# Kernel optimization log

Hardware: AMD Instinct MI355X
Metric: run time of the kernel (lower is better)

## Reference

```python
import jax, jax.numpy as jnp
import numpy as np

N, NB, D, F, E, NUM_RBF = 50000, 256, 128, 16, 800000, 15
EPS = 1e-7
NEG = 0.01
MAX_LEN = 5.0


def _glorot(k, shape):
    return jax.random.normal(k, shape, dtype=jnp.float32) / np.float32(np.sqrt(shape[0]))


def setup_inputs() -> dict:
    key = jax.random.key(0)
    ks = jax.random.split(key, 32)
    inp = {}
    inp['h_A'] = jax.random.normal(ks[0], (N, D), jnp.float32)
    inp['v_A'] = jax.random.normal(ks[1], (N, F, 3), jnp.float32)
    inp['x_A'] = jax.random.normal(ks[2], (N, 3), jnp.float32) * 3.0
    inp['h_B'] = jax.random.normal(ks[3], (NB, D), jnp.float32)
    inp['mask'] = jnp.ones((N, NB), jnp.float32)
    inp['src'] = jax.random.randint(ks[4], (E,), 0, N, dtype=jnp.int32)
    inp['dst'] = jax.random.randint(ks[5], (E,), 0, N, dtype=jnp.int32)
    inp['rbf_k'] = jnp.array([0.5], jnp.float32)
    inp['W_rbf1'] = _glorot(ks[6], (NUM_RBF, D)); inp['b_rbf1'] = jnp.zeros((D,), jnp.float32)
    inp['W_rbf2'] = _glorot(ks[7], (NUM_RBF, F)); inp['b_rbf2'] = jnp.zeros((F,), jnp.float32)
    inp['W_rbf3'] = _glorot(ks[8], (NUM_RBF, F)); inp['b_rbf3'] = jnp.zeros((F,), jnp.float32)
    inp['vn1_W'] = _glorot(ks[9], (F, F)); inp['vn1_U'] = _glorot(ks[10], (F, F))
    inp['vn2_W'] = _glorot(ks[11], (F, F)); inp['vn2_U'] = _glorot(ks[12], (F, F))
    inp['vn3_W'] = _glorot(ks[13], (F, F)); inp['vn3_U'] = _glorot(ks[14], (F, F))
    inp['phi1_W'] = _glorot(ks[15], (D + F, D)); inp['phi1_b'] = jnp.zeros((D,), jnp.float32)
    inp['phi2_W'] = _glorot(ks[16], (D + F, F)); inp['phi2_b'] = jnp.zeros((F,), jnp.float32)
    inp['phi3_W'] = _glorot(ks[17], (D, F)); inp['phi3_b'] = jnp.zeros((F,), jnp.float32)
    inp['Wq'] = _glorot(ks[18], (D, D)); inp['Wk'] = _glorot(ks[19], (D, D))
    inp['Wv'] = _glorot(ks[20], (D, D)); inp['bv'] = jnp.zeros((D,), jnp.float32)
    inp['gru_Wih'] = _glorot(ks[21], (3 * D, 2 * D)) * 0.5
    inp['gru_Whh'] = _glorot(ks[22], (3 * D, D)) * 0.5
    inp['gru_bih'] = jnp.zeros((3 * D,), jnp.float32)
    inp['gru_bhh'] = jnp.zeros((3 * D,), jnp.float32)
    inp['vmlp_W1'] = _glorot(ks[23], (2 * F, 2 * F)); inp['vmlp_U1'] = _glorot(ks[24], (2 * F, 2 * F))
    inp['vmlp_W2'] = _glorot(ks[25], (F, 2 * F))
    return inp


def _forward(h_A, v_A, x_A, h_B, mask, src, dst, rbf_k, W_rbf1, b_rbf1, W_rbf2, b_rbf2,
             W_rbf3, b_rbf3, vn1_W, vn1_U, vn2_W, vn2_U, vn3_W, vn3_U, phi1_W, phi1_b,
             phi2_W, phi2_b, phi3_W, phi3_b, Wq, Wk, Wv, bv, gru_Wih, gru_Whh, gru_bih,
             gru_bhh, vmlp_W1, vmlp_U1, vmlp_W2):
    lrelu = lambda x: jax.nn.leaky_relu(x, NEG)

    def vn_relu(v, W, U):  # Vector Neuron linear + VN-ReLU; v: [n, f, 3]
        q = jnp.einsum('gf,nfc->ngc', W, v)
        k = jnp.einsum('gf,nfc->ngc', U, v)
        dot = jnp.sum(q * k, -1, keepdims=True)
        ksq = jnp.sum(k * k, -1, keepdims=True) + EPS
        return jnp.where(dot >= 0, q, q - (dot / ksq) * k)

    # --- per-node mixed scalar/vector features (generate_mixed_features) ---
    vnorm1 = jnp.linalg.norm(vn_relu(v_A, vn1_W, vn1_U), axis=2) + EPS  # [N,F]
    vnorm2 = jnp.linalg.norm(vn_relu(v_A, vn2_W, vn2_U), axis=2) + EPS
    hp = lrelu(jnp.concatenate([h_A, vnorm1], 1) @ phi1_W + phi1_b)     # [N,D]
    hpp = lrelu(jnp.concatenate([h_A, vnorm2], 1) @ phi2_W + phi2_b)    # [N,F]
    vp = vn_relu(v_A, vn3_W, vn3_U) * lrelu(h_A @ phi3_W + phi3_b)[:, :, None]  # [N,F,3]

    # --- cross attention A <- B ---
    q = lrelu(h_A @ Wq)
    kk = lrelu(h_B @ Wk)
    vv = h_B @ Wv + bv
    a = mask * (q @ kk.T) - 1000.0 * (1.0 - mask)                       # [N,NB]
    attn = jax.nn.softmax(a, axis=1) @ vv                               # [N,D]

    # --- edge-wise RBF expansion + point convolution messages ---
    r_ij = x_A[src] - x_A[dst]                                          # [E,3]
    rnorm = jnp.linalg.norm(r_ij, axis=1, keepdims=True)                # [E,1]
    centers = jnp.linspace(0.0, MAX_LEN, NUM_RBF, dtype=jnp.float32)
    rbf = jnp.exp(-jnp.square(rnorm - centers) * rbf_k)                 # [E,R]
    rbf_h = rbf @ W_rbf1 + b_rbf1                                       # [E,D]
    rbf_v1 = rbf @ W_rbf2 + b_rbf2                                      # [E,F]
    rbf_v2 = rbf @ W_rbf3 + b_rbf3                                      # [E,F]
    msg_h = rbf_h * hp[dst]                                             # [E,D]
    # einsum('ef,ef,ec->efc', rbf_v2, hpp_dst, r_ij)
    msg_v = rbf_v1[:, :, None] * vp[dst] + (rbf_v2 * hpp[dst])[:, :, None] * r_ij[:, None, :]

    # --- mean aggregation at destination nodes (update_all copy_e + mean) ---
    n_nodes = h_A.shape[0]
    cnt = jax.ops.segment_sum(jnp.ones((src.shape[0],), msg_h.dtype), dst, num_segments=n_nodes)
    den = jnp.maximum(cnt, 1.0)
    agg_h = jax.ops.segment_sum(msg_h, dst, num_segments=n_nodes) / den[:, None]
    agg_v = jax.ops.segment_sum(msg_v, dst, num_segments=n_nodes) / den[:, None, None]

    # --- GRUCell(2D, D): input = [h, cross_attn], hidden = aggregated message ---
    x_in = jnp.concatenate([h_A, attn], -1)                             # [N,2D]
    gi = x_in @ gru_Wih.T + gru_bih
    gh = agg_h @ gru_Whh.T + gru_bhh
    Dh = h_A.shape[1]
    r = jax.nn.sigmoid(gi[:, :Dh] + gh[:, :Dh])
    z = jax.nn.sigmoid(gi[:, Dh:2 * Dh] + gh[:, Dh:2 * Dh])
    n = jnp.tanh(gi[:, 2 * Dh:] + r * gh[:, 2 * Dh:])
    node_upd = h_A + ((1.0 - z) * n + z * agg_h)

    # --- vector update via Vector_MLP(2F -> F) with residual ---
    vin = jnp.concatenate([v_A, agg_v], axis=1)                         # [N,2F,3]
    vh = vn_relu(vin, vmlp_W1, vmlp_U1)
    v_evolved = v_A + jnp.einsum('gf,nfc->ngc', vmlp_W2, vh)            # [N,F,3]
    return v_evolved, node_upd


def reference(h_A, v_A, x_A, h_B, mask, src, dst, rbf_k, W_rbf1, b_rbf1, W_rbf2, b_rbf2,
              W_rbf3, b_rbf3, vn1_W, vn1_U, vn2_W, vn2_U, vn3_W, vn3_U, phi1_W, phi1_b,
              phi2_W, phi2_b, phi3_W, phi3_b, Wq, Wk, Wv, bv, gru_Wih, gru_Whh, gru_bih,
              gru_bhh, vmlp_W1, vmlp_U1, vmlp_W2):
    return _forward(h_A, v_A, x_A, h_B, mask, src, dst, rbf_k, W_rbf1, b_rbf1, W_rbf2,
                    b_rbf2, W_rbf3, b_rbf3, vn1_W, vn1_U, vn2_W, vn2_U, vn3_W, vn3_U,
                    phi1_W, phi1_b, phi2_W, phi2_b, phi3_W, phi3_b, Wq, Wk, Wv, bv,
                    gru_Wih, gru_Whh, gru_bih, gru_bhh, vmlp_W1, vmlp_U1, vmlp_W2)
```

## Files before the change

kernel.cpp:

```cpp
#include <hip/hip_runtime.h>
#include <math.h>

#define NN 50000
#define NBB 256
#define DD 128
#define FF 16
#define EE 800000
#define RR 15
#define EPSV 1e-7f
#define CSPACE (5.0f/14.0f)

__device__ __forceinline__ float lrelu(float x){ return x >= 0.f ? x : 0.01f*x; }
__device__ __forceinline__ float sigmoidf_(float x){ return 1.f/(1.f+expf(-x)); }

typedef __bf16 bf16x8 __attribute__((ext_vector_type(8)));
typedef float f32x4 __attribute__((ext_vector_type(4)));

__device__ __forceinline__ unsigned short f2bf(float x){
    union { float f; unsigned int u; } a; a.f = x;
    unsigned int r = (a.u + 0x7fffu + ((a.u >> 16) & 1u)) >> 16;
    return (unsigned short)r;
}
__device__ __forceinline__ unsigned int pack2(float a, float b){
    return (unsigned int)f2bf(a) | ((unsigned int)f2bf(b) << 16);
}
__device__ __forceinline__ float bf2f(unsigned short v){
    union { unsigned int u; float f; } a; a.u = ((unsigned int)v) << 16; return a.f;
}
__device__ __forceinline__ bf16x8 ld8(const unsigned short* p){
    union { uint4 u; bf16x8 b; } x; x.u = *(const uint4*)p; return x.b;
}

__global__ void k_prep(const float* __restrict__ Wih, const float* __restrict__ Whh,
                       const float* __restrict__ Wq,
                       const float* __restrict__ phi1W, const float* __restrict__ phi2W,
                       const float* __restrict__ phi3W,
                       const float* __restrict__ Wr1, const float* __restrict__ br1,
                       unsigned short* __restrict__ pWih, unsigned short* __restrict__ pWhh,
                       unsigned short* __restrict__ pWq,
                       unsigned short* __restrict__ pPhi1, unsigned short* __restrict__ pPhi2,
                       unsigned short* __restrict__ pPhi3, unsigned short* __restrict__ pWr1){
    int i = blockIdx.x*256 + threadIdx.x;
    if (i < 3*8*8*64*8){
        int e = i&7, l=(i>>3)&63, kt=(i>>9)&7, c=(i>>12)&7, q=i>>15;
        int row = q*128 + c*16 + (l&15);
        int k = kt*32 + (l>>4)*8 + e;
        pWih[i] = f2bf(Wih[row*256 + k]);
    }
    if (i < 3*8*4*64*8){
        int e = i&7, l=(i>>3)&63, kt=(i>>9)&3, c=(i>>11)&7, q=i>>14;
        int row = q*128 + c*16 + (l&15);
        int k = kt*32 + (l>>4)*8 + e;
        pWhh[i] = f2bf(Whh[row*128 + k]);
    }
    if (i < 8*4*64*8){
        int e = i&7, l=(i>>3)&63, kt=(i>>9)&3, c=(i>>11)&7;
        pWq[i] = f2bf(Wq[(kt*32 + (l>>4)*8 + e)*DD + c*16 + (l&15)]);
    }
    if (i < 8*5*64*8){
        int e = i&7, l=(i>>3)&63;
        int t = i>>9;
        int kt = t%5, c = t/5;
        int k = kt*32 + (l>>4)*8 + e;
        int col = c*16 + (l&15);
        pPhi1[i] = f2bf(k < 144 ? phi1W[k*DD + col] : 0.f);
    }
    if (i < 5*64*8){
        int e = i&7, l=(i>>3)&63, kt = i>>9;
        int k = kt*32 + (l>>4)*8 + e;
        int col = l&15;
        pPhi2[i] = f2bf(k < 144 ? phi2W[k*FF + col] : 0.f);
    }
    if (i < 4*64*8){
        int e = i&7, l=(i>>3)&63, kt = i>>9;
        int k = kt*32 + (l>>4)*8 + e;
        int col = l&15;
        pPhi3[i] = f2bf(phi3W[k*FF + col]);
    }
    if (i < 8*64*8){
        int e = i&7, l=(i>>3)&63, c = i>>9;
        int col = c*16 + (l&15);
        int k = (l>>4)*8 + e;
        float v = 0.f;
        if (k == 0) v = br1[col];
        else if (k < 16) v = Wr1[(k-1)*DD + col];
        pWr1[i] = f2bf(v);
    }
}

__global__ __launch_bounds__(512) void k_node(
    const float* __restrict__ hA, const float* __restrict__ vA,
    const float* __restrict__ vn1W, const float* __restrict__ vn1U,
    const float* __restrict__ vn2W, const float* __restrict__ vn2U,
    const float* __restrict__ vn3W, const float* __restrict__ vn3U,
    const unsigned short* __restrict__ pPhi1, const float* __restrict__ phi1b,
    const unsigned short* __restrict__ pPhi2, const float* __restrict__ phi2b,
    const unsigned short* __restrict__ pPhi3, const float* __restrict__ phi3b,
    float* __restrict__ hpO, float* __restrict__ hppO, float* __restrict__ vpO)
{
    __shared__ unsigned short sH[64*128];
    __shared__ unsigned short sE[64*64];
    __shared__ float sVA[64*48];
    __shared__ float sO3[64*16*3];
    __shared__ float sW[6*256];
    int tid = threadIdx.x;
    int n0 = blockIdx.x*64;

    #pragma unroll
    for (int it = 0; it < 2; ++it){
        int c = tid + it*512;
        int row = c >> 4, cb = c & 15;
        int gn = n0 + row; if (gn > NN-1) gn = NN-1;
        const float* p = hA + (size_t)gn*DD + cb*8;
        float4 f0 = *(const float4*)p;
        float4 f1 = *(const float4*)(p+4);
        uint4 u;
        u.x = pack2(f0.x,f0.y); u.y = pack2(f0.z,f0.w);
        u.z = pack2(f1.x,f1.y); u.w = pack2(f1.z,f1.w);
        *(uint4*)&sH[row*128 + ((cb ^ (row&7))*8)] = u;
    }
    #pragma unroll
    for (int it = 0; it < 6; ++it){
        int i = tid + it*512;
        int row = i/48, cc = i%48;
        int gn = n0 + row; if (gn > NN-1) gn = NN-1;
        sVA[i] = vA[(size_t)gn*48 + cc];
    }
    #pragma unroll
    for (int it = 0; it < 3; ++it){
        int i = tid + it*512;
        float v;
        if      (i <  256) v = vn1W[i];
        else if (i <  512) v = vn1U[i-256];
        else if (i <  768) v = vn2W[i-512];
        else if (i < 1024) v = vn2U[i-768];
        else if (i < 1280) v = vn3W[i-1024];
        else               v = vn3U[i-1280];
        sW[i] = v;
    }
    {
        uint2* z = (uint2*)sE;
        z[tid] = make_uint2(0u,0u);
        z[tid+512] = make_uint2(0u,0u);
    }
    __syncthreads();

    #pragma unroll
    for (int it = 0; it < 2; ++it){
        int item = tid + it*512;
        int nl = item >> 4, g = item & 15;
        const float* v = &sVA[nl*48];
        float q0[3]={0,0,0}, q1[3]={0,0,0}, q2[3]={0,0,0};
        float c0[3]={0,0,0}, c1[3]={0,0,0}, c2[3]={0,0,0};
        #pragma unroll
        for (int ff = 0; ff < FF; ++ff){
            int fi = (ff + g) & 15;
            float v0 = v[fi*3], v1 = v[fi*3+1], v2 = v[fi*3+2];
            #pragma unroll
            for (int m = 0; m < 3; ++m){
                float w = sW[m*512 + g*16 + fi];
                float u = sW[m*512 + 256 + g*16 + fi];
                q0[m] += w*v0; q1[m] += w*v1; q2[m] += w*v2;
                c0[m] += u*v0; c1[m] += u*v1; c2[m] += u*v2;
            }
        }
        #pragma unroll
        for (int m = 0; m < 3; ++m){
            float dot = q0[m]*c0[m] + q1[m]*c1[m] + q2[m]*c2[m];
            float ksq = c0[m]*c0[m] + c1[m]*c1[m] + c2[m]*c2[m] + EPSV;
            float s = dot >= 0.f ? 0.f : dot/ksq;
            float o0 = q0[m]-s*c0[m], o1 = q1[m]-s*c1[m], o2 = q2[m]-s*c2[m];
            if (m < 2){
                float nr = sqrtf(o0*o0+o1*o1+o2*o2) + EPSV;
                int col = (m==0) ? g : (32+g);
                int cb = col>>3;
                sE[nl*64 + ((cb ^ (nl&7))*8) + (col&7)] = f2bf(nr);
            } else {
                float* o = &sO3[(nl*16+g)*3];
                o[0]=o0; o[1]=o1; o[2]=o2;
            }
        }
    }
    __syncthreads();

    int wv = tid>>6, l = tid&63, lr = l&15, lg = l>>4;

    f32x4 a1[4];
    #pragma unroll
    for (int rt = 0; rt < 4; ++rt) a1[rt] = (f32x4){0.f,0.f,0.f,0.f};
    for (int kt = 0; kt < 4; ++kt){
        bf16x8 b = ld8(pPhi1 + ((size_t)(wv*5+kt)*64 + l)*8);
        #pragma unroll
        for (int rt = 0; rt < 4; ++rt){
            int row = rt*16 + lr;
            bf16x8 a = ld8(&sH[row*128 + (((kt*4+lg) ^ (row&7))*8)]);
            a1[rt] = __builtin_amdgcn_mfma_f32_16x16x32_bf16(a, b, a1[rt], 0, 0, 0);
        }
    }
    {
        bf16x8 b = ld8(pPhi1 + ((size_t)(wv*5+4)*64 + l)*8);
        #pragma unroll
        for (int rt = 0; rt < 4; ++rt){
            int row = rt*16 + lr;
            bf16x8 a = ld8(&sE[row*64 + ((lg ^ (row&7))*8)]);
            a1[rt] = __builtin_amdgcn_mfma_f32_16x16x32_bf16(a, b, a1[rt], 0, 0, 0);
        }
    }
    f32x4 a23 = (f32x4){0.f,0.f,0.f,0.f};
    if (wv < 4){
        int row = wv*16 + lr;
        for (int kt = 0; kt < 4; ++kt){
            bf16x8 b = ld8(pPhi3 + ((size_t)kt*64 + l)*8);
            bf16x8 a = ld8(&sH[row*128 + (((kt*4+lg) ^ (row&7))*8)]);
            a23 = __builtin_amdgcn_mfma_f32_16x16x32_bf16(a, b, a23, 0, 0, 0);
        }
    } else {
        int row = (wv-4)*16 + lr;
        for (int kt = 0; kt < 4; ++kt){
            bf16x8 b = ld8(pPhi2 + ((size_t)kt*64 + l)*8);
            bf16x8 a = ld8(&sH[row*128 + (((kt*4+lg) ^ (row&7))*8)]);
            a23 = __builtin_amdgcn_mfma_f32_16x16x32_bf16(a, b, a23, 0, 0, 0);
        }
        {
            bf16x8 b = ld8(pPhi2 + ((size_t)4*64 + l)*8);
            bf16x8 a = ld8(&sE[row*64 + (((4+lg) ^ (row&7))*8)]);
            a23 = __builtin_amdgcn_mfma_f32_16x16x32_bf16(a, b, a23, 0, 0, 0);
        }
    }

    {
        int col = wv*16 + lr;
        float b1 = phi1b[col];
        #pragma unroll
        for (int rt = 0; rt < 4; ++rt){
            #pragma unroll
            for (int r4 = 0; r4 < 4; ++r4){
                int n = n0 + rt*16 + lg*4 + r4;
                if (n < NN) hpO[(size_t)n*DD + col] = lrelu(a1[rt][r4] + b1);
            }
        }
    }
    if (wv < 4){
        float b3 = phi3b[lr];
        #pragma unroll
        for (int r4 = 0; r4 < 4; ++r4){
            int nl = wv*16 + lg*4 + r4;
            int n = n0 + nl;
            float gate = lrelu(a23[r4] + b3);
            if (n < NN){
                const float* o = &sO3[(nl*16+lr)*3];
                float* vo = vpO + (size_t)n*48 + lr*3;
                vo[0] = o[0]*gate; vo[1] = o[1]*gate; vo[2] = o[2]*gate;
            }
        }
    } else {
        float b2 = phi2b[lr];
        #pragma unroll
        for (int r4 = 0; r4 < 4; ++r4){
            int nl = (wv-4)*16 + lg*4 + r4;
            int n = n0 + nl;
            if (n < NN) hppO[(size_t)n*FF + lr] = lrelu(a23[r4] + b2);
        }
    }
}

__global__ __launch_bounds__(128) void k_kv(
    const float* __restrict__ hB, const float* __restrict__ Wk,
    const float* __restrict__ Wv, const float* __restrict__ bv,
    unsigned short* __restrict__ pKK, unsigned short* __restrict__ pVV)
{
    __shared__ float sB[DD];
    int b = blockIdx.x, j = threadIdx.x;
    sB[j] = hB[(size_t)b*DD + j];
    __syncthreads();
    float ak = 0.f, av = bv[j];
    for (int i = 0; i < DD; ++i){
        float h = sB[i];
        ak += h*Wk[i*DD+j];
        av += h*Wv[i*DD+j];
    }
    {
        int c = b>>4, lr = b&15, kt = j>>5, lg = (j>>3)&3, e = j&7;
        pKK[((c*4+kt)*64 + lg*16 + lr)*8 + e] = f2bf(lrelu(ak));
    }
    {
        int kt = b>>5, lg = (b>>3)&3, e = b&7, c = j>>4, lr = j&15;
        pVV[((c*8+kt)*64 + lg*16 + lr)*8 + e] = f2bf(av);
    }
}

__global__ __launch_bounds__(512, 4) void k_attn_mfma(
    const float* __restrict__ hA, const unsigned short* __restrict__ pWq,
    const unsigned short* __restrict__ pKK, const unsigned short* __restrict__ pVV,
    const float* __restrict__ mask, float* __restrict__ attnO)
{
    __shared__ unsigned short sU[64*256];
    __shared__ float sMx[64][2];
    __shared__ float sSm[64][2];
    unsigned short* sX = sU;
    unsigned short* sQ = sU + 64*128;
    unsigned short* sP = sU;
    int tid = threadIdx.x;
    int n0 = blockIdx.x*64;

    #pragma unroll
    for (int it = 0; it < 2; ++it){
        int c = tid + it*512;
        int row = c >> 4, cb = c & 15;
        int gn = n0 + row; if (gn > NN-1) gn = NN-1;
        const float* srcp = hA + (size_t)gn*DD + cb*8;
        float4 f0 = *(const float4*)srcp;
        float4 f1 = *(const float4*)(srcp+4);
        uint4 u;
        u.x = pack2(f0.x,f0.y); u.y = pack2(f0.z,f0.w);
        u.z = pack2(f1.x,f1.y); u.w = pack2(f1.z,f1.w);
        *(uint4*)&sX[row*128 + ((cb ^ (row&7))*8)] = u;
    }
    __syncthreads();

    int wv = tid>>6, l = tid&63, lr = l&15, lg = l>>4;
    int rw = wv>>1, chh = wv&1;
    int rowA = rw*16 + lr;

    {
        f32x4 q[4];
        #pragma unroll
        for (int c = 0; c < 4; ++c) q[c] = (f32x4){0.f,0.f,0.f,0.f};
        for (int kt = 0; kt < 4; ++kt){
            bf16x8 a = ld8(&sX[rowA*128 + (((kt*4+lg) ^ (rowA&7))*8)]);
            #pragma unroll
            for (int c = 0; c < 4; ++c){
                bf16x8 b = ld8(pWq + (size_t)(((chh*4+c)*4 + kt)*512) + l*8);
                q[c] = __builtin_amdgcn_mfma_f32_16x16x32_bf16(a, b, q[c], 0, 0, 0);
            }
        }
        __syncthreads();
        #pragma unroll
        for (int c = 0; c < 4; ++c)
        #pragma unroll
        for (int r4 = 0; r4 < 4; ++r4){
            int row = rw*16 + lg*4 + r4;
            int col = chh*64 + c*16 + lr;
            int cb = col>>3;
            sQ[row*128 + ((cb ^ (row&7))*8) + (col&7)] = f2bf(lrelu(q[c][r4]));
        }
    }
    __syncthreads();

    f32x4 S[8];
    #pragma unroll
    for (int cl = 0; cl < 8; ++cl) S[cl] = (f32x4){0.f,0.f,0.f,0.f};
    for (int kt = 0; kt < 4; ++kt){
        bf16x8 a = ld8(&sQ[rowA*128 + (((kt*4+lg) ^ (rowA&7))*8)]);
        #pragma unroll
        for (int cl = 0; cl < 8; ++cl){
            bf16x8 b = ld8(pKK + (size_t)(((chh*8+cl)*4 + kt)*512) + l*8);
            S[cl] = __builtin_amdgcn_mfma_f32_16x16x32_bf16(a, b, S[cl], 0, 0, 0);
        }
    }
    float den[4];
    #pragma unroll
    for (int r4 = 0; r4 < 4; ++r4){
        int row = rw*16 + lg*4 + r4;
        int gn = n0 + row; if (gn > NN-1) gn = NN-1;
        float mx = -1e30f;
        #pragma unroll
        for (int cl = 0; cl < 8; ++cl){
            int col = chh*128 + cl*16 + lr;
            float m = mask[(size_t)gn*NBB + col];
            float s = m*S[cl][r4] - 1000.f*(1.f-m);
            S[cl][r4] = s;
            mx = fmaxf(mx, s);
        }
        mx = fmaxf(mx, __shfl_xor(mx, 1));
        mx = fmaxf(mx, __shfl_xor(mx, 2));
        mx = fmaxf(mx, __shfl_xor(mx, 4));
        mx = fmaxf(mx, __shfl_xor(mx, 8));
        if (lr == 0) sMx[row][chh] = mx;
    }
    __syncthreads();
    #pragma unroll
    for (int r4 = 0; r4 < 4; ++r4){
        int row = rw*16 + lg*4 + r4;
        float m = fmaxf(sMx[row][0], sMx[row][1]);
        float sm = 0.f;
        #pragma unroll
        for (int cl = 0; cl < 8; ++cl){
            float p = expf(S[cl][r4] - m);
            S[cl][r4] = p;
            sm += p;
        }
        sm += __shfl_xor(sm, 1);
        sm += __shfl_xor(sm, 2);
        sm += __shfl_xor(sm, 4);
        sm += __shfl_xor(sm, 8);
        if (lr == 0) sSm[row][chh] = sm;
    }
    __syncthreads();
    #pragma unroll
    for (int r4 = 0; r4 < 4; ++r4){
        int row = rw*16 + lg*4 + r4;
        den[r4] = sSm[row][0] + sSm[row][1];
    }
    #pragma unroll
    for (int cl = 0; cl < 8; ++cl)
    #pragma unroll
    for (int r4 = 0; r4 < 4; ++r4){
        int row = rw*16 + lg*4 + r4;
        int col = chh*128 + cl*16 + lr;
        int cb = col>>3;
        sP[row*256 + ((cb ^ (row&7))*8) + (col&7)] = f2bf(S[cl][r4]);
    }
    __syncthreads();

    f32x4 O[4];
    #pragma unroll
    for (int c = 0; c < 4; ++c) O[c] = (f32x4){0.f,0.f,0.f,0.f};
    for (int kt = 0; kt < 8; ++kt){
        bf16x8 a = ld8(&sP[rowA*256 + (((kt*4+lg) ^ (rowA&7))*8)]);
        #pragma unroll
        for (int c = 0; c < 4; ++c){
            bf16x8 b = ld8(pVV + (size_t)(((chh*4+c)*8 + kt)*512) + l*8);
            O[c] = __builtin_amdgcn_mfma_f32_16x16x32_bf16(a, b, O[c], 0, 0, 0);
        }
    }
    #pragma unroll
    for (int c = 0; c < 4; ++c)
    #pragma unroll
    for (int r4 = 0; r4 < 4; ++r4){
        int row = rw*16 + lg*4 + r4;
        int n = n0 + row;
        if (n < NN){
            int col = chh*64 + c*16 + lr;
            attnO[(size_t)n*DD + col] = O[c][r4] / den[r4];
        }
    }
}

__global__ __launch_bounds__(256) void k_hist(const int* __restrict__ dst, int* __restrict__ deg){
    int e = blockIdx.x*256 + threadIdx.x;
    if (e < EE) atomicAdd(&deg[dst[e]], 1);
}

__global__ __launch_bounds__(256) void k_scan1(const int* __restrict__ deg,
                                               int* __restrict__ excl, int* __restrict__ bsum){
    __shared__ int s[256];
    int tid = threadIdx.x;
    int i = blockIdx.x*256 + tid;
    int v = (i < NN) ? deg[i] : 0;
    s[tid] = v;
    __syncthreads();
    for (int o = 1; o < 256; o <<= 1){
        int t = 0;
        if (tid >= o) t = s[tid-o];
        __syncthreads();
        if (tid >= o) s[tid] += t;
        __syncthreads();
    }
    if (i < NN) excl[i] = s[tid] - v;
    if (tid == 255) bsum[blockIdx.x] = s[255];
}

__global__ __launch_bounds__(256) void k_scan2(const int* __restrict__ bsum,
                                               int* __restrict__ boff, int nb){
    __shared__ int s[256];
    int tid = threadIdx.x;
    int v = (tid < nb) ? bsum[tid] : 0;
    s[tid] = v;
    __syncthreads();
    for (int o = 1; o < 256; o <<= 1){
        int t = 0;
        if (tid >= o) t = s[tid-o];
        __syncthreads();
        if (tid >= o) s[tid] += t;
        __syncthreads();
    }
    if (tid < nb) boff[tid] = s[tid] - v;
}

__global__ __launch_bounds__(256) void k_scan3(const int* __restrict__ excl,
                                               const int* __restrict__ boff,
                                               int* __restrict__ start, int* __restrict__ cursor){
    int i = blockIdx.x*256 + threadIdx.x;
    if (i < NN){
        int st = excl[i] + boff[blockIdx.x];
        start[i] = st;
        cursor[i] = st;
    }
    if (i == 0) start[NN] = EE;
}

__global__ __launch_bounds__(256) void k_scatter(const int* __restrict__ src,
                                                 const int* __restrict__ dst,
                                                 int* __restrict__ cursor, int* __restrict__ esrc){
    int e = blockIdx.x*256 + threadIdx.x;
    if (e >= EE) return;
    int pos = atomicAdd(&cursor[dst[e]], 1);
    esrc[pos] = src[e];
}

__global__ __launch_bounds__(256) void k_gather(const int* __restrict__ start,
                                                const int* __restrict__ esrc,
                                                const float* __restrict__ xA,
                                                const float* __restrict__ rbf_k,
                                                float* __restrict__ acc)
{
    int gt = blockIdx.x*256 + threadIdx.x;
    int n = gt >> 2, sub = gt & 3;
    if (n >= NN) return;
    float kc = rbf_k[0];
    float xd0 = xA[n*3+0], xd1 = xA[n*3+1], xd2 = xA[n*3+2];
    float a[64];
    #pragma unroll
    for (int i = 0; i < 64; ++i) a[i] = 0.f;
    int b0 = start[n], b1 = start[n+1];
    for (int i = b0 + sub; i < b1; i += 4){
        int s = esrc[i];
        float r0 = xA[s*3+0]-xd0, r1 = xA[s*3+1]-xd1, r2 = xA[s*3+2]-xd2;
        float rn = sqrtf(r0*r0+r1*r1+r2*r2);
        a[0] += 1.f;
        a[16] += r0; a[17] += r1; a[18] += r2;
        #pragma unroll
        for (int q = 0; q < RR; ++q){
            float df = rn - (float)q*CSPACE;
            float rb = expf(-df*df*kc);
            a[1+q] += rb;
            a[19+q*3+0] += rb*r0;
            a[19+q*3+1] += rb*r1;
            a[19+q*3+2] += rb*r2;
        }
    }
    #pragma unroll
    for (int i = 0; i < 64; ++i){
        a[i] += __shfl_xor(a[i], 1);
        a[i] += __shfl_xor(a[i], 2);
    }
    float4* o = (float4*)(acc + (size_t)n*64);
    #pragma unroll
    for (int i = 0; i < 4; ++i){
        int idx = sub*4 + i;
        o[idx] = make_float4(a[4*idx], a[4*idx+1], a[4*idx+2], a[4*idx+3]);
    }
}

__global__ __launch_bounds__(512) void k_gru_mfma(
    const float* __restrict__ hA, const float* __restrict__ attn,
    const float* __restrict__ hp, const float* __restrict__ acc,
    const unsigned short* __restrict__ pWr1,
    const unsigned short* __restrict__ pWih, const unsigned short* __restrict__ pWhh,
    const float* __restrict__ bih, const float* __restrict__ bhh,
    float* __restrict__ outNode)
{
    __shared__ unsigned short sX[64*256];
    __shared__ unsigned short sGm[64*128];
    __shared__ unsigned short sM[64*32];
    int tid = threadIdx.x;
    int n0 = blockIdx.x*64;

    #pragma unroll
    for (int it = 0; it < 4; ++it){
        int c = tid + it*512;
        int row = c >> 5, cb = c & 31;
        int gn = n0 + row; if (gn > NN-1) gn = NN-1;
        int k = cb*8;
        const float* srcp = (k < DD) ? (hA + (size_t)gn*DD + k)
                                     : (attn + (size_t)gn*DD + (k-DD));
        float4 f0 = *(const float4*)srcp;
        float4 f1 = *(const float4*)(srcp+4);
        uint4 u;
        u.x = pack2(f0.x,f0.y); u.y = pack2(f0.z,f0.w);
        u.z = pack2(f1.x,f1.y); u.w = pack2(f1.z,f1.w);
        *(uint4*)&sX[row*256 + ((cb ^ (row&7))*8)] = u;
    }
    #pragma unroll
    for (int it = 0; it < 4; ++it){
        int i = tid + it*512;
        int row = i >> 5, k = i & 31;
        int gn = n0 + row; if (gn > NN-1) gn = NN-1;
        float v = (k < 16) ? acc[(size_t)gn*64 + k] : 0.f;
        sM[i] = f2bf(v);
    }
    __syncthreads();

    int wv = tid >> 6, l = tid & 63;
    int lr = l & 15, lg = l >> 4;
    int col = wv*16 + lr;

    {
        f32x4 sv[4];
        #pragma unroll
        for (int rt = 0; rt < 4; ++rt) sv[rt] = (f32x4){0.f,0.f,0.f,0.f};
        bf16x8 b = ld8(pWr1 + (size_t)wv*512 + l*8);
        #pragma unroll
        for (int rt = 0; rt < 4; ++rt){
            int row = rt*16 + lr;
            bf16x8 a = ld8(&sM[row*32 + lg*8]);
            sv[rt] = __builtin_amdgcn_mfma_f32_16x16x32_bf16(a, b, sv[rt], 0, 0, 0);
        }
        #pragma unroll
        for (int rt = 0; rt < 4; ++rt){
            #pragma unroll
            for (int r4 = 0; r4 < 4; ++r4){
                int row = rt*16 + lg*4 + r4;
                int gn = n0 + row; if (gn > NN-1) gn = NN-1;
                float cnt = bf2f(sM[row*32]);
                float den = fmaxf(cnt, 1.f);
                float g = hp[(size_t)gn*DD + col] * sv[rt][r4] / den;
                sGm[row*128 + (((col>>3) ^ (row&7))*8) + (col&7)] = f2bf(g);
            }
        }
    }
    __syncthreads();

    f32x4 aR[4], aZ[4], aNI[4], aNH[4];
    #pragma unroll
    for (int rt = 0; rt < 4; ++rt){
        aR[rt] = (f32x4){0.f,0.f,0.f,0.f};
        aZ[rt] = (f32x4){0.f,0.f,0.f,0.f};
        aNI[rt] = (f32x4){0.f,0.f,0.f,0.f};
        aNH[rt] = (f32x4){0.f,0.f,0.f,0.f};
    }
    const unsigned short* bR = pWih + ((size_t)(0*8 + wv)*8)*512 + l*8;
    const unsigned short* bZ = pWih + ((size_t)(1*8 + wv)*8)*512 + l*8;
    const unsigned short* bN = pWih + ((size_t)(2*8 + wv)*8)*512 + l*8;
    for (int kt = 0; kt < 8; ++kt){
        bf16x8 br_ = ld8(bR + kt*512);
        bf16x8 bz_ = ld8(bZ + kt*512);
        bf16x8 bn_ = ld8(bN + kt*512);
        #pragma unroll
        for (int rt = 0; rt < 4; ++rt){
            int rowA = rt*16 + lr;
            bf16x8 a = ld8(&sX[rowA*256 + (((kt*4 + lg) ^ (rowA&7))*8)]);
            aR[rt]  = __builtin_amdgcn_mfma_f32_16x16x32_bf16(a, br_, aR[rt], 0, 0, 0);
            aZ[rt]  = __builtin_amdgcn_mfma_f32_16x16x32_bf16(a, bz_, aZ[rt], 0, 0, 0);
            aNI[rt] = __builtin_amdgcn_mfma_f32_16x16x32_bf16(a, bn_, aNI[rt], 0, 0, 0);
        }
    }
    const unsigned short* cR = pWhh + ((size_t)(0*8 + wv)*4)*512 + l*8;
    const unsigned short* cZ = pWhh + ((size_t)(1*8 + wv)*4)*512 + l*8;
    const unsigned short* cN = pWhh + ((size_t)(2*8 + wv)*4)*512 + l*8;
    for (int kt = 0; kt < 4; ++kt){
        bf16x8 br_ = ld8(cR + kt*512);
        bf16x8 bz_ = ld8(cZ + kt*512);
        bf16x8 bn_ = ld8(cN + kt*512);
        #pragma unroll
        for (int rt = 0; rt < 4; ++rt){
            int rowA = rt*16 + lr;
            bf16x8 a = ld8(&sGm[rowA*128 + (((kt*4 + lg) ^ (rowA&7))*8)]);
            aR[rt]  = __builtin_amdgcn_mfma_f32_16x16x32_bf16(a, br_, aR[rt], 0, 0, 0);
            aZ[rt]  = __builtin_amdgcn_mfma_f32_16x16x32_bf16(a, bz_, aZ[rt], 0, 0, 0);
            aNH[rt] = __builtin_amdgcn_mfma_f32_16x16x32_bf16(a, bn_, aNH[rt], 0, 0, 0);
        }
    }

    float b_r = bih[col] + bhh[col];
    float b_z = bih[DD+col] + bhh[DD+col];
    float b_ni = bih[2*DD+col];
    float b_nh = bhh[2*DD+col];
    #pragma unroll
    for (int rt = 0; rt < 4; ++rt){
        #pragma unroll
        for (int r4 = 0; r4 < 4; ++r4){
            int nl = rt*16 + lg*4 + r4;
            int n = n0 + nl;
            if (n < NN){
                float rg = sigmoidf_(aR[rt][r4] + b_r);
                float zg = sigmoidf_(aZ[rt][r4] + b_z);
                float ng = tanhf(aNI[rt][r4] + b_ni + rg*(aNH[rt][r4] + b_nh));
                float sg = bf2f(sGm[nl*128 + (((col>>3) ^ (nl&7))*8) + (col&7)]);
                float h = bf2f(sX[nl*256 + (((col>>3) ^ (nl&7))*8) + (col&7)]);
                outNode[(size_t)n*DD + col] = h + (1.f-zg)*ng + zg*sg;
            }
        }
    }
}

__global__ __launch_bounds__(256) void k_vec(
    const float* __restrict__ vA, const float* __restrict__ vp,
    const float* __restrict__ hpp, const float* __restrict__ acc,
    const float* __restrict__ Wr2, const float* __restrict__ br2,
    const float* __restrict__ Wr3, const float* __restrict__ br3,
    const float* __restrict__ W1, const float* __restrict__ U1,
    const float* __restrict__ W2, float* __restrict__ outV)
{
    __shared__ float sW1[32*32], sU1[32*32], sW2[16*32];
    __shared__ float sWr2[RR*FF], sWr3[RR*FF];
    __shared__ float sVin[8][32][3];
    __shared__ float sVh[8][32][3];
    __shared__ float sAcc[8][64];
    __shared__ float sVA[8][48];
    int tid = threadIdx.x;
    for (int i = tid; i < 1024; i += 256){ sW1[i]=W1[i]; sU1[i]=U1[i]; }
    for (int i = tid; i < 512; i += 256) sW2[i]=W2[i];
    for (int i = tid; i < RR*FF; i += 256){ sWr2[i]=Wr2[i]; sWr3[i]=Wr3[i]; }
    int n0 = blockIdx.x*8;
    for (int i = tid; i < 8*64; i += 256) sAcc[i/64][i%64] = acc[(size_t)n0*64 + i];
    for (int i = tid; i < 8*48; i += 256) sVA[i/48][i%48] = vA[(size_t)n0*48 + i];
    __syncthreads();
    int t = tid >> 5, g = tid & 31;
    int n = n0 + t;
    if (g < 16){
        int f = g;
        float cnt = sAcc[t][0];
        float den = fmaxf(cnt, 1.f);
        float s1 = cnt*br2[f];
        #pragma unroll
        for (int r = 0; r < RR; ++r) s1 += sAcc[t][1+r]*sWr2[r*FF+f];
        float hpv = hpp[(size_t)n*FF+f];
        float b3 = br3[f];
        #pragma unroll
        for (int c = 0; c < 3; ++c){
            float s2 = b3*sAcc[t][16+c];
            #pragma unroll
            for (int r = 0; r < RR; ++r) s2 += sAcc[t][19+r*3+c]*sWr3[r*FF+f];
            float aggv = (vp[(size_t)n*48 + f*3 + c]*s1 + hpv*s2)/den;
            sVin[t][FF+f][c] = aggv;
            sVin[t][f][c] = sVA[t][f*3+c];
        }
    }
    __syncthreads();
    {
        float q0=0,q1=0,q2=0,k0=0,k1=0,k2=0;
        #pragma unroll
        for (int ff = 0; ff < 32; ++ff){
            int f = (ff + g) & 31;
            float w = sW1[g*32+f], u = sU1[g*32+f];
            float v0=sVin[t][f][0], v1=sVin[t][f][1], v2=sVin[t][f][2];
            q0+=w*v0;q1+=w*v1;q2+=w*v2;
            k0+=u*v0;k1+=u*v1;k2+=u*v2;
        }
        float dot=q0*k0+q1*k1+q2*k2;
        float ksq=k0*k0+k1*k1+k2*k2+EPSV;
        float s = dot>=0.f?0.f:dot/ksq;
        sVh[t][g][0]=q0-s*k0; sVh[t][g][1]=q1-s*k1; sVh[t][g][2]=q2-s*k2;
    }
    __syncthreads();
    if (g < 16){
        float o0=sVA[t][g*3+0], o1=sVA[t][g*3+1], o2=sVA[t][g*3+2];
        #pragma unroll
        for (int ff = 0; ff < 32; ++ff){
            int f = (ff + g) & 31;
            float w = sW2[g*32+f];
            o0 += w*sVh[t][f][0];
            o1 += w*sVh[t][f][1];
            o2 += w*sVh[t][f][2];
        }
        outV[(size_t)n*48 + g*3 + 0] = o0;
        outV[(size_t)n*48 + g*3 + 1] = o1;
        outV[(size_t)n*48 + g*3 + 2] = o2;
    }
}

extern "C" void kernel_launch(void* const* d_in, const int* in_sizes, int n_in,
                              void* d_out, int out_size, void* d_ws, size_t ws_size,
                              hipStream_t stream)
{
    const float* hA   = (const float*)d_in[0];
    const float* vA   = (const float*)d_in[1];
    const float* xA   = (const float*)d_in[2];
    const float* hB   = (const float*)d_in[3];
    const float* mask = (const float*)d_in[4];
    const int*   src  = (const int*)d_in[5];
    const int*   dst  = (const int*)d_in[6];
    const float* rbfk = (const float*)d_in[7];
    const float* Wr1  = (const float*)d_in[8];
    const float* br1  = (const float*)d_in[9];
    const float* Wr2  = (const float*)d_in[10];
    const float* br2  = (const float*)d_in[11];
    const float* Wr3  = (const float*)d_in[12];
    const float* br3  = (const float*)d_in[13];
    const float* vn1W = (const float*)d_in[14];
    const float* vn1U = (const float*)d_in[15];
    const float* vn2W = (const float*)d_in[16];
    const float* vn2U = (const float*)d_in[17];
    const float* vn3W = (const float*)d_in[18];
    const float* vn3U = (const float*)d_in[19];
    const float* phi1W= (const float*)d_in[20];
    const float* phi1b= (const float*)d_in[21];
    const float* phi2W= (const float*)d_in[22];
    const float* phi2b= (const float*)d_in[23];
    const float* phi3W= (const float*)d_in[24];
    const float* phi3b= (const float*)d_in[25];
    const float* Wq   = (const float*)d_in[26];
    const float* Wk   = (const float*)d_in[27];
    const float* Wv   = (const float*)d_in[28];
    const float* bv   = (const float*)d_in[29];
    const float* Wih  = (const float*)d_in[30];
    const float* Whh  = (const float*)d_in[31];
    const float* bih  = (const float*)d_in[32];
    const float* bhh  = (const float*)d_in[33];
    const float* W1   = (const float*)d_in[34];
    const float* U1   = (const float*)d_in[35];
    const float* W2   = (const float*)d_in[36];

    float* ws = (float*)d_ws;
    float* hp     = ws;  ws += (size_t)NN*DD;
    float* hpp    = ws;  ws += (size_t)NN*FF;
    float* vp     = ws;  ws += (size_t)NN*FF*3;
    float* attn   = ws;  ws += (size_t)NN*DD;
    float* acc    = ws;  ws += (size_t)NN*64;
    unsigned short* pWih = (unsigned short*)ws; ws += (size_t)3*8*8*512/2;
    unsigned short* pWhh = (unsigned short*)ws; ws += (size_t)3*8*4*512/2;
    unsigned short* pWq  = (unsigned short*)ws; ws += (size_t)8*4*512/2;
    unsigned short* pKK  = (unsigned short*)ws; ws += (size_t)16*4*512/2;
    unsigned short* pVV  = (unsigned short*)ws; ws += (size_t)8*8*512/2;
    unsigned short* pPhi1= (unsigned short*)ws; ws += (size_t)8*5*512/2;
    unsigned short* pPhi2= (unsigned short*)ws; ws += (size_t)5*512/2;
    unsigned short* pPhi3= (unsigned short*)ws; ws += (size_t)4*512/2;
    unsigned short* pWr1 = (unsigned short*)ws; ws += (size_t)8*512/2;
    int* deg    = (int*)ws;  ws += NN;
    int* excl   = (int*)ws;  ws += NN;
    int* bsum   = (int*)ws;  ws += 256;
    int* boff   = (int*)ws;  ws += 256;
    int* startN = (int*)ws;  ws += NN+1;
    int* cursor = (int*)ws;  ws += NN;
    int* esrc   = (int*)ws;  ws += EE;

    float* outV = (float*)d_out;
    float* outH = (float*)d_out + (size_t)NN*FF*3;

    const int NB_SCAN = (NN + 255)/256;

    hipMemsetAsync(deg, 0, (size_t)NN*sizeof(int), stream);
    k_prep<<<384, 256, 0, stream>>>(Wih, Whh, Wq, phi1W, phi2W, phi3W, Wr1, br1,
                                    pWih, pWhh, pWq, pPhi1, pPhi2, pPhi3, pWr1);
    k_hist<<<(EE+255)/256, 256, 0, stream>>>(dst, deg);
    k_scan1<<<NB_SCAN, 256, 0, stream>>>(deg, excl, bsum);
    k_scan2<<<1, 256, 0, stream>>>(bsum, boff, NB_SCAN);
    k_scan3<<<NB_SCAN, 256, 0, stream>>>(excl, boff, startN, cursor);
    k_scatter<<<(EE+255)/256, 256, 0, stream>>>(src, dst, cursor, esrc);
    k_gather<<<(NN*4+255)/256, 256, 0, stream>>>(startN, esrc, xA, rbfk, acc);
    k_node<<<(NN+63)/64, 512, 0, stream>>>(hA, vA, vn1W, vn1U, vn2W, vn2U, vn3W, vn3U,
                                           pPhi1, phi1b, pPhi2, phi2b, pPhi3, phi3b,
                                           hp, hpp, vp);
    k_kv<<<NBB, 128, 0, stream>>>(hB, Wk, Wv, bv, pKK, pVV);
    k_attn_mfma<<<(NN+63)/64, 512, 0, stream>>>(hA, pWq, pKK, pVV, mask, attn);
    k_gru_mfma<<<(NN+63)/64, 512, 0, stream>>>(hA, attn, hp, acc, pWr1,
                                               pWih, pWhh, bih, bhh, outH);
    k_vec<<<NN/8, 256, 0, stream>>>(vA, vp, hpp, acc, Wr2, br2, Wr3, br3, W1, U1, W2, outV);
}
```

Measured before the change: 344.1 us.

## Store attention and phi1 intermediates as bf16 with pre-swizzled tiled attention layout

k_node now writes the hp intermediate as bf16 instead of fp32. k_attn_mfma stages its output through shared memory and writes it as a bf16 tile image already in the swizzled layout that k_gru_mfma loads directly into its shared tile. Together this halves the intermediate HBM traffic between kernels and removes the fp32-to-bf16 conversion for the attention half of the GRU input. The sM buffer is padded to a stride of 40 to reduce LDS bank conflicts. The cost is extra syncs and an LDS round trip in the attention epilogue, plus bf16 rounding of hp before its multiply in GRU.

After: 346.3 us. Within noise of the previous version (+0.6%).

```diff
diff --git a/kernel.cpp b/kernel.cpp
--- a/kernel.cpp
+++ b/kernel.cpp
@@ -9,6 +9,7 @@
 #define RR 15
 #define EPSV 1e-7f
 #define CSPACE (5.0f/14.0f)
+#define NBLK 782
 
 __device__ __forceinline__ float lrelu(float x){ return x >= 0.f ? x : 0.01f*x; }
 __device__ __forceinline__ float sigmoidf_(float x){ return 1.f/(1.f+expf(-x)); }
@@ -96,7 +97,7 @@
     const unsigned short* __restrict__ pPhi1, const float* __restrict__ phi1b,
     const unsigned short* __restrict__ pPhi2, const float* __restrict__ phi2b,
     const unsigned short* __restrict__ pPhi3, const float* __restrict__ phi3b,
-    float* __restrict__ hpO, float* __restrict__ hppO, float* __restrict__ vpO)
+    unsigned short* __restrict__ hpB, float* __restrict__ hppO, float* __restrict__ vpO)
 {
     __shared__ unsigned short sH[64*128];
     __shared__ unsigned short sE[64*64];
@@ -236,7 +237,7 @@
             #pragma unroll
             for (int r4 = 0; r4 < 4; ++r4){
                 int n = n0 + rt*16 + lg*4 + r4;
-                if (n < NN) hpO[(size_t)n*DD + col] = lrelu(a1[rt][r4] + b1);
+                if (n < NN) hpB[(size_t)n*DD + col] = f2bf(lrelu(a1[rt][r4] + b1));
             }
         }
     }
@@ -292,7 +293,7 @@
 __global__ __launch_bounds__(512, 4) void k_attn_mfma(
     const float* __restrict__ hA, const unsigned short* __restrict__ pWq,
     const unsigned short* __restrict__ pKK, const unsigned short* __restrict__ pVV,
-    const float* __restrict__ mask, float* __restrict__ attnO)
+    const float* __restrict__ mask, unsigned short* __restrict__ attnB)
 {
     __shared__ unsigned short sU[64*256];
     __shared__ float sMx[64][2];
@@ -300,6 +301,7 @@
     unsigned short* sX = sU;
     unsigned short* sQ = sU + 64*128;
     unsigned short* sP = sU;
+    unsigned short* sImg = sU;
     int tid = threadIdx.x;
     int n0 = blockIdx.x*64;
 
@@ -424,16 +426,20 @@
             O[c] = __builtin_amdgcn_mfma_f32_16x16x32_bf16(a, b, O[c], 0, 0, 0);
         }
     }
+    __syncthreads();
     #pragma unroll
     for (int c = 0; c < 4; ++c)
     #pragma unroll
     for (int r4 = 0; r4 < 4; ++r4){
         int row = rw*16 + lg*4 + r4;
-        int n = n0 + row;
-        if (n < NN){
-            int col = chh*64 + c*16 + lr;
-            attnO[(size_t)n*DD + col] = O[c][r4] / den[r4];
-        }
+        int col = chh*64 + c*16 + lr;
+        sImg[row*128 + (((col>>3) ^ (row&7))*8) + (col&7)] = f2bf(O[c][r4] / den[r4]);
+    }
+    __syncthreads();
+    #pragma unroll
+    for (int it = 0; it < 2; ++it){
+        int i = tid + it*512;
+        ((uint4*)attnB)[(size_t)blockIdx.x*1024 + i] = ((const uint4*)sImg)[i];
     }
 }
 
@@ -544,8 +550,8 @@
 }
 
 __global__ __launch_bounds__(512) void k_gru_mfma(
-    const float* __restrict__ hA, const float* __restrict__ attn,
-    const float* __restrict__ hp, const float* __restrict__ acc,
+    const float* __restrict__ hA, const unsigned short* __restrict__ attnB,
+    const unsigned short* __restrict__ hpB, const float* __restrict__ acc,
     const unsigned short* __restrict__ pWr1,
     const unsigned short* __restrict__ pWih, const unsigned short* __restrict__ pWhh,
     const float* __restrict__ bih, const float* __restrict__ bhh,
@@ -553,18 +559,16 @@
 {
     __shared__ unsigned short sX[64*256];
     __shared__ unsigned short sGm[64*128];
-    __shared__ unsigned short sM[64*32];
+    __shared__ unsigned short sM[64*40];
     int tid = threadIdx.x;
     int n0 = blockIdx.x*64;
 
     #pragma unroll
-    for (int it = 0; it < 4; ++it){
+    for (int it = 0; it < 2; ++it){
         int c = tid + it*512;
-        int row = c >> 5, cb = c & 31;
+        int row = c >> 4, cb = c & 15;
         int gn = n0 + row; if (gn > NN-1) gn = NN-1;
-        int k = cb*8;
-        const float* srcp = (k < DD) ? (hA + (size_t)gn*DD + k)
-                                     : (attn + (size_t)gn*DD + (k-DD));
+        const float* srcp = hA + (size_t)gn*DD + cb*8;
         float4 f0 = *(const float4*)srcp;
         float4 f1 = *(const float4*)(srcp+4);
         uint4 u;
@@ -573,12 +577,19 @@
         *(uint4*)&sX[row*256 + ((cb ^ (row&7))*8)] = u;
     }
     #pragma unroll
+    for (int it = 0; it < 2; ++it){
+        int i = tid + it*512;
+        uint4 v = ((const uint4*)attnB)[(size_t)blockIdx.x*1024 + i];
+        int row = i >> 4, p = i & 15;
+        *(uint4*)&sX[row*256 + 128 + p*8] = v;
+    }
+    #pragma unroll
     for (int it = 0; it < 4; ++it){
         int i = tid + it*512;
         int row = i >> 5, k = i & 31;
         int gn = n0 + row; if (gn > NN-1) gn = NN-1;
         float v = (k < 16) ? acc[(size_t)gn*64 + k] : 0.f;
-        sM[i] = f2bf(v);
+        sM[row*40 + k] = f2bf(v);
     }
     __syncthreads();
 
@@ -594,7 +605,7 @@
         #pragma unroll
         for (int rt = 0; rt < 4; ++rt){
             int row = rt*16 + lr;
-            bf16x8 a = ld8(&sM[row*32 + lg*8]);
+            bf16x8 a = ld8(&sM[row*40 + lg*8]);
             sv[rt] = __builtin_amdgcn_mfma_f32_16x16x32_bf16(a, b, sv[rt], 0, 0, 0);
         }
         #pragma unroll
@@ -603,9 +614,9 @@
             for (int r4 = 0; r4 < 4; ++r4){
                 int row = rt*16 + lg*4 + r4;
                 int gn = n0 + row; if (gn > NN-1) gn = NN-1;
-                float cnt = bf2f(sM[row*32]);
+                float cnt = bf2f(sM[row*40]);
                 float den = fmaxf(cnt, 1.f);
-                float g = hp[(size_t)gn*DD + col] * sv[rt][r4] / den;
+                float g = bf2f(hpB[(size_t)gn*DD + col]) * sv[rt][r4] / den;
                 sGm[row*128 + (((col>>3) ^ (row&7))*8) + (col&7)] = f2bf(g);
             }
         }
@@ -794,10 +805,10 @@
     const float* W2   = (const float*)d_in[36];
 
     float* ws = (float*)d_ws;
-    float* hp     = ws;  ws += (size_t)NN*DD;
+    unsigned short* hpB = (unsigned short*)ws; ws += (size_t)NN*DD/2;
+    unsigned short* attnB = (unsigned short*)ws; ws += ((size_t)NBLK*64*128)/2;
     float* hpp    = ws;  ws += (size_t)NN*FF;
     float* vp     = ws;  ws += (size_t)NN*FF*3;
-    float* attn   = ws;  ws += (size_t)NN*DD;
     float* acc    = ws;  ws += (size_t)NN*64;
     unsigned short* pWih = (unsigned short*)ws; ws += (size_t)3*8*8*512/2;
     unsigned short* pWhh = (unsigned short*)ws; ws += (size_t)3*8*4*512/2;
@@ -830,12 +841,12 @@
     k_scan3<<<NB_SCAN, 256, 0, stream>>>(excl, boff, startN, cursor);
     k_scatter<<<(EE+255)/256, 256, 0, stream>>>(src, dst, cursor, esrc);
     k_gather<<<(NN*4+255)/256, 256, 0, stream>>>(startN, esrc, xA, rbfk, acc);
-    k_node<<<(NN+63)/64, 512, 0, stream>>>(hA, vA, vn1W, vn1U, vn2W, vn2U, vn3W, vn3U,
-                                           pPhi1, phi1b, pPhi2, phi2b, pPhi3, phi3b,
-                                           hp, hpp, vp);
+    k_node<<<NBLK, 512, 0, stream>>>(hA, vA, vn1W, vn1U, vn2W, vn2U, vn3W, vn3U,
+                                     pPhi1, phi1b, pPhi2, phi2b, pPhi3, phi3b,
+                                     hpB, hpp, vp);
     k_kv<<<NBB, 128, 0, stream>>>(hB, Wk, Wv, bv, pKK, pVV);
-    k_attn_mfma<<<(NN+63)/64, 512, 0, stream>>>(hA, pWq, pKK, pVV, mask, attn);
-    k_gru_mfma<<<(NN+63)/64, 512, 0, stream>>>(hA, attn, hp, acc, pWr1,
-                                               pWih, pWhh, bih, bhh, outH);
+    k_attn_mfma<<<NBLK, 512, 0, stream>>>(hA, pWq, pKK, pVV, mask, attnB);
+    k_gru_mfma<<<NBLK, 512, 0, stream>>>(hA, attnB, hpB, acc, pWr1,
+                                         pWih, pWhh, bih, bhh, outH);
     k_vec<<<NN/8, 256, 0, stream>>>(vA, vp, hpp, acc, Wr2, br2, Wr3, br3, W1, U1, W2, outV);
 }
```
